# Performance work log

Measured on AMD Instinct MI355X. Metric: run time of the kernel, lower is better.

Reference implementation:

```python
import jax, jax.numpy as jnp
import numpy as np

OUT_SIZE = 7        # output_size (7, 7)
RATIO = 2           # RoIAlign sampling_ratio
FINEST = 56.0       # finest_scale
SCALES = (0.25, 0.125, 0.0625, 0.03125)  # FPN spatial scales, strides 4/8/16/32
IMG_H, IMG_W = 800, 1216
NUM_ROIS = 1024


def _roi_align(feat, rois, scale):
    """RoIAlign (torchvision legacy, aligned=False) for one level.
    feat: [C, H, W]; rois: [4, K] xyxy in image coords. Returns [K, C, 7, 7]."""
    C, H, W = feat.shape
    K = rois.shape[1]
    x1, y1, x2, y2 = rois * scale
    roi_w = jnp.maximum(x2 - x1, 1.0)
    roi_h = jnp.maximum(y2 - y1, 1.0)
    S = OUT_SIZE * RATIO  # 14 sample points per spatial dim
    g = (jnp.arange(S, dtype=feat.dtype) + 0.5) / RATIO  # offsets in bin units
    ys = y1[:, None] + g[None, :] * (roi_h / OUT_SIZE)[:, None]  # [K, S]
    xs = x1[:, None] + g[None, :] * (roi_w / OUT_SIZE)[:, None]  # [K, S]
    # points outside [-1, H]x[-1, W] contribute 0 (torchvision semantics)
    vy = (ys >= -1.0) & (ys <= H)
    vx = (xs >= -1.0) & (xs <= W)
    valid = vy[:, :, None] & vx[:, None, :]  # [K, S, S]
    y = jnp.clip(ys, 0.0, H - 1)
    x = jnp.clip(xs, 0.0, W - 1)
    y0f = jnp.floor(y)
    x0f = jnp.floor(x)
    y0 = y0f.astype(jnp.int32)
    x0 = x0f.astype(jnp.int32)
    yh = jnp.minimum(y0 + 1, H - 1)
    xh = jnp.minimum(x0 + 1, W - 1)
    wy = (y - y0f)[:, None, :, None]  # [K,1,S,1]
    wx = (x - x0f)[:, None, None, :]  # [K,1,1,S]
    ff = feat.reshape(C, H * W)

    def gather(yi, xi):  # yi,xi: [K,S] -> [K,C,S,S]
        idx = yi[:, :, None] * W + xi[:, None, :]  # [K,S,S]
        return jnp.transpose(ff[:, idx], (1, 0, 2, 3))

    v00 = gather(y0, x0)
    v01 = gather(y0, xh)
    v10 = gather(yh, x0)
    v11 = gather(yh, xh)
    val = (v00 * (1.0 - wy) * (1.0 - wx) + v01 * (1.0 - wy) * wx
           + v10 * wy * (1.0 - wx) + v11 * wy * wx)
    val = val * valid[:, None, :, :].astype(val.dtype)
    # average the RATIO x RATIO samples per output bin
    out = val.reshape(K, C, OUT_SIZE, RATIO, OUT_SIZE, RATIO).mean(axis=(3, 5))
    return out


def _map_levels(rois, n_lvls):
    scale = jnp.sqrt((rois[2] - rois[0] + 1.0) * (rois[3] - rois[1] + 1.0))
    lv = jnp.floor(jnp.log2(scale / FINEST + 1e-6))
    return jnp.clip(lv, 0, n_lvls - 1).astype(jnp.int32)


def setup_inputs() -> dict:
    key = jax.random.key(0)
    ks = jax.random.split(key, 8)
    feat0 = jax.random.normal(ks[0], (256, 200, 304), dtype=jnp.float32)
    feat1 = jax.random.normal(ks[1], (256, 100, 152), dtype=jnp.float32)
    feat2 = jax.random.normal(ks[2], (256, 50, 76), dtype=jnp.float32)
    feat3 = jax.random.normal(ks[3], (256, 25, 38), dtype=jnp.float32)
    cx = jax.random.uniform(ks[4], (NUM_ROIS,), minval=0.0, maxval=float(IMG_W))
    cy = jax.random.uniform(ks[5], (NUM_ROIS,), minval=0.0, maxval=float(IMG_H))
    w = jnp.exp(jax.random.uniform(ks[6], (NUM_ROIS,), minval=np.log(16.0), maxval=np.log(640.0)))
    h = jnp.exp(jax.random.uniform(ks[7], (NUM_ROIS,), minval=np.log(16.0), maxval=np.log(640.0)))
    x1 = jnp.clip(cx - w / 2, 0.0, IMG_W - 1.0)
    x2 = jnp.clip(cx + w / 2, 0.0, IMG_W - 1.0)
    y1 = jnp.clip(cy - h / 2, 0.0, IMG_H - 1.0)
    y2 = jnp.clip(cy + h / 2, 0.0, IMG_H - 1.0)
    rois = jnp.stack([x1, y1, x2, y2]).astype(jnp.float32)  # [4, K]
    return {"feat0": feat0, "feat1": feat1, "feat2": feat2, "feat3": feat3, "rois": rois}


def reference(feat0, feat1, feat2, feat3, rois):
    feats = (feat0, feat1, feat2, feat3)
    n_lvls = len(feats)
    tar = _map_levels(rois, n_lvls)  # [K] target FPN level per RoI
    K = rois.shape[1]
    C = feat0.shape[0]
    out = jnp.zeros((K, C, OUT_SIZE, OUT_SIZE), dtype=feat0.dtype)
    for i in range(n_lvls):  # fixed small loop over structurally distinct levels
        lvl_out = _roi_align(feats[i], rois, SCALES[i])
        out = out + jnp.where((tar == i)[:, None, None, None], lvl_out, 0.0)
    return out
```

## Files before the change

### kernel.cpp

```cpp
#include <hip/hip_runtime.h>
#include <hip/hip_fp16.h>
#include <math.h>

#define OUTS 7
#define NBIN 49
#define NCH 256
#define LDSW 1200

#define O1 15564800ull
#define O2 19456000ull
#define O3 20428800ull
#define WS_FLOATS 20672000ull
#define WS_BYTES  (WS_FLOATS * 4ull)

__global__ __launch_bounds__(256) void transpose_cl(
    const float* __restrict__ f0, const float* __restrict__ f1,
    const float* __restrict__ f2, const float* __restrict__ f3,
    __half* __restrict__ ws)
{
    const int bt = blockIdx.x;
    const int cb = blockIdx.y * 64;
    const float* src; __half* dst; int HW, t0;
    if (bt < 950)       { src = f0; dst = ws;      HW = 60800; t0 = bt; }
    else if (bt < 1188) { src = f1; dst = ws + O1; HW = 15200; t0 = bt - 950; }
    else if (bt < 1248) { src = f2; dst = ws + O2; HW = 3800;  t0 = bt - 1188; }
    else                { src = f3; dst = ws + O3; HW = 950;   t0 = bt - 1248; }
    const int hw0 = t0 * 64;

    __shared__ float tile[64][65];
    const int tx = threadIdx.x & 63;
    const int ty = threadIdx.x >> 6;

#pragma unroll
    for (int j = 0; j < 16; ++j) {
        const int c = cb + ty + 4 * j;
        const int hw = hw0 + tx;
        tile[ty + 4 * j][tx] = (hw < HW) ? src[(size_t)c * HW + hw] : 0.0f;
    }
    __syncthreads();

    const int cp = threadIdx.x & 31;
    const int hh = threadIdx.x >> 5;
#pragma unroll
    for (int j = 0; j < 8; ++j) {
        const int hl = hh + 8 * j;
        const int hw = hw0 + hl;
        if (hw < HW) {
            const __half2 h = __floats2half2_rn(tile[2 * cp][hl], tile[2 * cp + 1][hl]);
            *(__half2*)(dst + (size_t)hw * 256 + cb + 2 * cp) = h;
        }
    }
}

__global__ __launch_bounds__(512) void roi_main(
    const __half* __restrict__ ws, const float* __restrict__ rois,
    float* __restrict__ out, int K)
{
    const int k = blockIdx.x;
    const int cbase = blockIdx.y * 128;
    const int tid = threadIdx.x;
    const int wid = tid >> 6;
    const int lane = tid & 63;

    const float rx1 = rois[0 * K + k];
    const float ry1 = rois[1 * K + k];
    const float rx2 = rois[2 * K + k];
    const float ry2 = rois[3 * K + k];

    const float sroi = sqrtf((rx2 - rx1 + 1.0f) * (ry2 - ry1 + 1.0f));
    int lv = (int)floorf(log2f(sroi / 56.0f + 1e-6f));
    lv = lv < 0 ? 0 : (lv > 3 ? 3 : lv);

    const __half* wb; int H, W; float sc;
    switch (lv) {
        case 0:  wb = ws;      H = 200; W = 304; sc = 0.25f;    break;
        case 1:  wb = ws + O1; H = 100; W = 152; sc = 0.125f;   break;
        case 2:  wb = ws + O2; H = 50;  W = 76;  sc = 0.0625f;  break;
        default: wb = ws + O3; H = 25;  W = 38;  sc = 0.03125f; break;
    }

    const float y1s = ry1 * sc;
    const float ystep = fmaxf(ry2 * sc - y1s, 1.0f) / (float)OUTS;
    const float x1s = rx1 * sc;
    const float xstep = fmaxf(rx2 * sc - x1s, 1.0f) / (float)OUTS;

    __shared__ int2   syo[14];  __shared__ float2 syw[14];
    __shared__ int2   sxo[14];  __shared__ float2 sxw[14];
    __shared__ __align__(16) float obuf[128 * NBIN];

    if (tid < 14) {
        const int s = tid;
        const float g = ((float)s + 0.5f) * 0.5f;
        const float ysv = y1s + g * ystep;
        const float v = (ysv >= -1.0f && ysv <= (float)H) ? 0.5f : 0.0f;
        const float y = fminf(fmaxf(ysv, 0.0f), (float)(H - 1));
        const float yf = floorf(y);
        const int y0 = (int)yf;
        const float wy = y - yf;
        syo[s] = make_int2(y0 * W, min(y0 + 1, H - 1) * W);
        syw[s] = make_float2((1.0f - wy) * v, wy * v);
    } else if (tid < 28) {
        const int s = tid - 14;
        const float g = ((float)s + 0.5f) * 0.5f;
        const float xsv = x1s + g * xstep;
        const float v = (xsv >= -1.0f && xsv <= (float)W) ? 0.5f : 0.0f;
        const float x = fminf(fmaxf(xsv, 0.0f), (float)(W - 1));
        const float xf = floorf(x);
        const int x0 = (int)xf;
        const float wx = x - xf;
        sxo[s] = make_int2(x0, min(x0 + 1, W - 1));
        sxw[s] = make_float2((1.0f - wx) * v, wx * v);
    }
    __syncthreads();

    const int half = lane >> 5;
    const int ch4 = (lane & 31) * 4;
    const __half* wbl = wb + cbase + ch4;

#pragma unroll
    for (int i = 0; i < 4; ++i) {
        const int bl = 2 * wid + 16 * i;
        if (bl > 48) break;
        const int b = bl + half;
        const int bc = b > 48 ? 48 : b;
        const int oh = bc / OUTS;
        const int ow = bc - oh * OUTS;

        const int2   ya = syo[2 * oh], yb = syo[2 * oh + 1];
        const float2 wa = syw[2 * oh], wbv = syw[2 * oh + 1];
        const int2   xa = sxo[2 * ow], xb = sxo[2 * ow + 1];
        const float2 ua = sxw[2 * ow], ub = sxw[2 * ow + 1];

        const int   yo[4] = { ya.x, ya.y, yb.x, yb.y };
        const float yw[4] = { wa.x, wa.y, wbv.x, wbv.y };
        const int   xo[4] = { xa.x, xa.y, xb.x, xb.y };
        const float xw[4] = { ua.x, ua.y, ub.x, ub.y };

        float a0 = 0.0f, a1 = 0.0f, a2 = 0.0f, a3 = 0.0f;
#pragma unroll
        for (int iy = 0; iy < 4; ++iy) {
#pragma unroll
            for (int ix = 0; ix < 4; ++ix) {
                const uint2 h2 = *(const uint2*)(wbl + ((size_t)(yo[iy] + xo[ix]) << 8));
                const float2 v0 = __half22float2(*(const __half2*)&h2.x);
                const float2 v1 = __half22float2(*(const __half2*)&h2.y);
                const float wv = yw[iy] * xw[ix];
                a0 += v0.x * wv;
                a1 += v0.y * wv;
                a2 += v1.x * wv;
                a3 += v1.y * wv;
            }
        }
        if (b < NBIN) {
            obuf[(ch4 + 0) * NBIN + b] = a0;
            obuf[(ch4 + 1) * NBIN + b] = a1;
            obuf[(ch4 + 2) * NBIN + b] = a2;
            obuf[(ch4 + 3) * NBIN + b] = a3;
        }
    }
    __syncthreads();

    const float4* o4 = (const float4*)obuf;
    float4* d4 = (float4*)(out + ((size_t)k * NCH + cbase) * NBIN);
    for (int i = tid; i < (128 * NBIN) / 4; i += 512) d4[i] = o4[i];
}

__global__ __launch_bounds__(256) void roi_extract_fallback(
    const float* __restrict__ f0, const float* __restrict__ f1,
    const float* __restrict__ f2, const float* __restrict__ f3,
    const float* __restrict__ rois, float* __restrict__ out, int K)
{
    const int k = blockIdx.x;
    if (k >= K) return;
    const int cbase = blockIdx.y * 32;
    const int tid = threadIdx.x;
    const int wid = tid >> 6;
    const int lane = tid & 63;
    const int bin = lane < NBIN ? lane : NBIN - 1;

    const float rx1 = rois[0 * K + k];
    const float ry1 = rois[1 * K + k];
    const float rx2 = rois[2 * K + k];
    const float ry2 = rois[3 * K + k];

    const float sroi = sqrtf((rx2 - rx1 + 1.0f) * (ry2 - ry1 + 1.0f));
    int lv = (int)floorf(log2f(sroi / 56.0f + 1e-6f));
    lv = lv < 0 ? 0 : (lv > 3 ? 3 : lv);

    const float* fbase; int H, W; float sc;
    switch (lv) {
        case 0:  fbase = f0; H = 200; W = 304; sc = 0.25f;    break;
        case 1:  fbase = f1; H = 100; W = 152; sc = 0.125f;   break;
        case 2:  fbase = f2; H = 50;  W = 76;  sc = 0.0625f;  break;
        default: fbase = f3; H = 25;  W = 38;  sc = 0.03125f; break;
    }
    const int HW = H * W;

    const float y1s = ry1 * sc;
    const float roih = fmaxf(ry2 * sc - y1s, 1.0f);
    const float x1s = rx1 * sc;
    const float roiw = fmaxf(rx2 * sc - x1s, 1.0f);
    const float ystep = roih / (float)OUTS;
    const float xstep = roiw / (float)OUTS;

    const float ysA = y1s + 0.25f * ystep, ysZ = y1s + 6.75f * ystep;
    const float xsA = x1s + 0.25f * xstep, xsZ = x1s + 6.75f * xstep;
    const int ylo = (int)floorf(fminf(fmaxf(ysA, 0.0f), (float)(H - 1)));
    const int xlo = (int)floorf(fminf(fmaxf(xsA, 0.0f), (float)(W - 1)));
    const int xhi = min((int)floorf(fminf(fmaxf(xsZ, 0.0f), (float)(W - 1))) + 1, W - 1);
    const int yhi = min((int)floorf(fminf(fmaxf(ysZ, 0.0f), (float)(H - 1))) + 1, H - 1);
    const int Ww = xhi - xlo + 1;
    const int Hw = yhi - ylo + 1;
    const int E = Ww * Hw;
    const bool useLds = (E <= LDSW);
    const int stride = useLds ? Ww : W;
    const int obase  = useLds ? 0 : (ylo * W + xlo);

    const int oh = bin / OUTS;
    const int ow = bin - oh * OUTS;

    int ry0[2], ry1i[2]; float wy[2], vy[2];
#pragma unroll
    for (int py = 0; py < 2; ++py) {
        const float g = ((float)(oh * 2 + py) + 0.5f) * 0.5f;
        const float ys = y1s + g * ystep;
        vy[py] = (ys >= -1.0f && ys <= (float)H) ? 1.0f : 0.0f;
        const float y = fminf(fmaxf(ys, 0.0f), (float)(H - 1));
        const float y0f = floorf(y);
        const int y0 = (int)y0f;
        ry0[py]  = y0 - ylo;
        ry1i[py] = min(y0 + 1, H - 1) - ylo;
        wy[py] = y - y0f;
    }
    int rx0[2], rx1i[2]; float wx[2], vx[2];
#pragma unroll
    for (int px = 0; px < 2; ++px) {
        const float g = ((float)(ow * 2 + px) + 0.5f) * 0.5f;
        const float xs = x1s + g * xstep;
        vx[px] = (xs >= -1.0f && xs <= (float)W) ? 1.0f : 0.0f;
        const float x = fminf(fmaxf(xs, 0.0f), (float)(W - 1));
        const float x0f = floorf(x);
        const int x0 = (int)x0f;
        rx0[px]  = x0 - xlo;
        rx1i[px] = min(x0 + 1, W - 1) - xlo;
        wx[px] = x - x0f;
    }

    int off[16]; float wt[16];
#pragma unroll
    for (int py = 0; py < 2; ++py) {
#pragma unroll
        for (int px = 0; px < 2; ++px) {
            const int i = (py * 2 + px) * 4;
            const float v = vy[py] * vx[px] * 0.25f;
            const float a = wy[py], b = wx[px];
            off[i + 0] = ry0[py]  * stride + rx0[px]  + obase; wt[i + 0] = (1.0f - a) * (1.0f - b) * v;
            off[i + 1] = ry0[py]  * stride + rx1i[px] + obase; wt[i + 1] = (1.0f - a) * b * v;
            off[i + 2] = ry1i[py] * stride + rx0[px]  + obase; wt[i + 2] = a * (1.0f - b) * v;
            off[i + 3] = ry1i[py] * stride + rx1i[px] + obase; wt[i + 3] = a * b * v;
        }
    }

    __shared__ float2 lds2[4 * LDSW];
    float2* const myw = &lds2[wid * LDSW];
    const float inv_Ww = 1.0f / (float)Ww;

#pragma unroll
    for (int j = 0; j < 4; ++j) {
        const int chA = cbase + wid * 8 + j * 2;
        const float* sA = fbase + (size_t)chA * HW + (size_t)ylo * W + xlo;
        const float* sB = sA + HW;

        if (useLds) {
            for (int e = lane; e < E; e += 64) {
                const int r = (int)(((float)e + 0.5f) * inv_Ww);
                const int g = r * W + (e - r * Ww);
                myw[e] = make_float2(sA[g], sB[g]);
            }
            if (lane < NBIN) {
                float ax = 0.0f, ay = 0.0f;
#pragma unroll
                for (int i = 0; i < 16; ++i) {
                    const float2 v = myw[off[i]];
                    ax += v.x * wt[i];
                    ay += v.y * wt[i];
                }
                float* outA = out + ((size_t)k * NCH + chA) * NBIN + bin;
                outA[0] = ax;
                outA[NBIN] = ay;
            }
        } else {
            if (lane < NBIN) {
                const float* pA = fbase + (size_t)chA * HW;
                const float* pB = pA + HW;
                float ax = 0.0f, ay = 0.0f;
#pragma unroll
                for (int i = 0; i < 16; ++i) {
                    ax += pA[off[i]] * wt[i];
                    ay += pB[off[i]] * wt[i];
                }
                float* outA = out + ((size_t)k * NCH + chA) * NBIN + bin;
                outA[0] = ax;
                outA[NBIN] = ay;
            }
        }
    }
}

extern "C" void kernel_launch(void* const* d_in, const int* in_sizes, int n_in,
                              void* d_out, int out_size, void* d_ws, size_t ws_size,
                              hipStream_t stream) {
    const float* f0 = (const float*)d_in[0];
    const float* f1 = (const float*)d_in[1];
    const float* f2 = (const float*)d_in[2];
    const float* f3 = (const float*)d_in[3];
    const float* rois = (const float*)d_in[4];
    float* out = (float*)d_out;
    int K = in_sizes[4] / 4;
    if (K <= 0) return;

    if (ws_size >= WS_BYTES) {
        __half* ws = (__half*)d_ws;
        transpose_cl<<<dim3(1263, 4), 256, 0, stream>>>(f0, f1, f2, f3, ws);
        roi_main<<<dim3(K, 2), 512, 0, stream>>>(ws, rois, out, K);
    } else {
        roi_extract_fallback<<<dim3(K, 8), 256, 0, stream>>>(f0, f1, f2, f3, rois, out, K);
    }
}
```

Before: 159.5 us.

## Vectorize transpose loads and process all channels per RoI block

The transpose kernel now reads float4 rows when a tile is fully in bounds and writes four half channels per store, with a padded LDS tile. roi_main drops the channel split, so one 512-thread block covers all 256 channels of a RoI, with each wave taking whole bins. The sample offsets are pre-multiplied by the channel stride, and all 16 gather loads are issued before accumulating to expose memory-level parallelism. The cost is a 50KB LDS output buffer per block, which lowers occupancy, and the grid is halved.

```diff
diff --git a/kernel.cpp b/kernel.cpp
--- a/kernel.cpp
+++ b/kernel.cpp
@@ -26,28 +26,43 @@
     else if (bt < 1248) { src = f2; dst = ws + O2; HW = 3800;  t0 = bt - 1188; }
     else                { src = f3; dst = ws + O3; HW = 950;   t0 = bt - 1248; }
     const int hw0 = t0 * 64;
-
-    __shared__ float tile[64][65];
-    const int tx = threadIdx.x & 63;
-    const int ty = threadIdx.x >> 6;
-
-#pragma unroll
-    for (int j = 0; j < 16; ++j) {
-        const int c = cb + ty + 4 * j;
-        const int hw = hw0 + tx;
-        tile[ty + 4 * j][tx] = (hw < HW) ? src[(size_t)c * HW + hw] : 0.0f;
+    const int tid = threadIdx.x;
+
+    __shared__ float tile[64][68];
+
+    const bool fast = ((HW & 3) == 0) && (hw0 + 64 <= HW);
+    if (fast) {
+#pragma unroll
+        for (int j = 0; j < 4; ++j) {
+            const int cl = (tid >> 4) + 16 * j;
+            const int h4 = (tid & 15) * 4;
+            const float4 v = *(const float4*)(src + (size_t)(cb + cl) * HW + hw0 + h4);
+            *(float4*)&tile[cl][h4] = v;
+        }
+    } else {
+        const int tx = tid & 63;
+        const int ty = tid >> 6;
+#pragma unroll
+        for (int j = 0; j < 16; ++j) {
+            const int c = cb + ty + 4 * j;
+            const int hw = hw0 + tx;
+            tile[ty + 4 * j][tx] = (hw < HW) ? src[(size_t)c * HW + hw] : 0.0f;
+        }
     }
     __syncthreads();
 
-    const int cp = threadIdx.x & 31;
-    const int hh = threadIdx.x >> 5;
-#pragma unroll
-    for (int j = 0; j < 8; ++j) {
-        const int hl = hh + 8 * j;
+#pragma unroll
+    for (int j = 0; j < 4; ++j) {
+        const int hl = (tid >> 4) + 16 * j;
         const int hw = hw0 + hl;
         if (hw < HW) {
-            const __half2 h = __floats2half2_rn(tile[2 * cp][hl], tile[2 * cp + 1][hl]);
-            *(__half2*)(dst + (size_t)hw * 256 + cb + 2 * cp) = h;
+            const int q = (tid & 15) * 4;
+            const __half2 h0 = __floats2half2_rn(tile[q + 0][hl], tile[q + 1][hl]);
+            const __half2 h1 = __floats2half2_rn(tile[q + 2][hl], tile[q + 3][hl]);
+            uint2 u;
+            u.x = *(const unsigned int*)&h0;
+            u.y = *(const unsigned int*)&h1;
+            *(uint2*)(dst + (size_t)hw * 256 + cb + q) = u;
         }
     }
 }
@@ -57,7 +72,6 @@
     float* __restrict__ out, int K)
 {
     const int k = blockIdx.x;
-    const int cbase = blockIdx.y * 128;
     const int tid = threadIdx.x;
     const int wid = tid >> 6;
     const int lane = tid & 63;
@@ -86,7 +100,7 @@
 
     __shared__ int2   syo[14];  __shared__ float2 syw[14];
     __shared__ int2   sxo[14];  __shared__ float2 sxw[14];
-    __shared__ __align__(16) float obuf[128 * NBIN];
+    __shared__ __align__(16) float obuf[NCH * NBIN];
 
     if (tid < 14) {
         const int s = tid;
@@ -97,7 +111,7 @@
         const float yf = floorf(y);
         const int y0 = (int)yf;
         const float wy = y - yf;
-        syo[s] = make_int2(y0 * W, min(y0 + 1, H - 1) * W);
+        syo[s] = make_int2(y0 * W * 256, min(y0 + 1, H - 1) * W * 256);
         syw[s] = make_float2((1.0f - wy) * v, wy * v);
     } else if (tid < 28) {
         const int s = tid - 14;
@@ -108,42 +122,45 @@
         const float xf = floorf(x);
         const int x0 = (int)xf;
         const float wx = x - xf;
-        sxo[s] = make_int2(x0, min(x0 + 1, W - 1));
+        sxo[s] = make_int2(x0 * 256, min(x0 + 1, W - 1) * 256);
         sxw[s] = make_float2((1.0f - wx) * v, wx * v);
     }
     __syncthreads();
 
-    const int half = lane >> 5;
-    const int ch4 = (lane & 31) * 4;
-    const __half* wbl = wb + cbase + ch4;
-
-#pragma unroll
-    for (int i = 0; i < 4; ++i) {
-        const int bl = 2 * wid + 16 * i;
-        if (bl > 48) break;
-        const int b = bl + half;
-        const int bc = b > 48 ? 48 : b;
-        const int oh = bc / OUTS;
-        const int ow = bc - oh * OUTS;
+    const int ch4 = lane * 4;
+    const __half* wbl = wb + ch4;
+
+    for (int b = wid; b < NBIN; b += 8) {
+        const int oh = b / OUTS;
+        const int ow = b - oh * OUTS;
 
         const int2   ya = syo[2 * oh], yb = syo[2 * oh + 1];
-        const float2 wa = syw[2 * oh], wbv = syw[2 * oh + 1];
+        const float2 wa = syw[2 * oh], wv2 = syw[2 * oh + 1];
         const int2   xa = sxo[2 * ow], xb = sxo[2 * ow + 1];
         const float2 ua = sxw[2 * ow], ub = sxw[2 * ow + 1];
 
         const int   yo[4] = { ya.x, ya.y, yb.x, yb.y };
-        const float yw[4] = { wa.x, wa.y, wbv.x, wbv.y };
+        const float yw[4] = { wa.x, wa.y, wv2.x, wv2.y };
         const int   xo[4] = { xa.x, xa.y, xb.x, xb.y };
         const float xw[4] = { ua.x, ua.y, ub.x, ub.y };
 
+        uint2 t[16];
+#pragma unroll
+        for (int iy = 0; iy < 4; ++iy) {
+#pragma unroll
+            for (int ix = 0; ix < 4; ++ix) {
+                t[iy * 4 + ix] = *(const uint2*)(wbl + (size_t)(yo[iy] + xo[ix]));
+            }
+        }
+
         float a0 = 0.0f, a1 = 0.0f, a2 = 0.0f, a3 = 0.0f;
 #pragma unroll
         for (int iy = 0; iy < 4; ++iy) {
 #pragma unroll
             for (int ix = 0; ix < 4; ++ix) {
-                const uint2 h2 = *(const uint2*)(wbl + ((size_t)(yo[iy] + xo[ix]) << 8));
-                const float2 v0 = __half22float2(*(const __half2*)&h2.x);
-                const float2 v1 = __half22float2(*(const __half2*)&h2.y);
+                const uint2 u = t[iy * 4 + ix];
+                const float2 v0 = __half22float2(*(const __half2*)&u.x);
+                const float2 v1 = __half22float2(*(const __half2*)&u.y);
                 const float wv = yw[iy] * xw[ix];
                 a0 += v0.x * wv;
                 a1 += v0.y * wv;
@@ -151,18 +168,16 @@
                 a3 += v1.y * wv;
             }
         }
-        if (b < NBIN) {
-            obuf[(ch4 + 0) * NBIN + b] = a0;
-            obuf[(ch4 + 1) * NBIN + b] = a1;
-            obuf[(ch4 + 2) * NBIN + b] = a2;
-            obuf[(ch4 + 3) * NBIN + b] = a3;
-        }
+        obuf[(ch4 + 0) * NBIN + b] = a0;
+        obuf[(ch4 + 1) * NBIN + b] = a1;
+        obuf[(ch4 + 2) * NBIN + b] = a2;
+        obuf[(ch4 + 3) * NBIN + b] = a3;
     }
     __syncthreads();
 
     const float4* o4 = (const float4*)obuf;
-    float4* d4 = (float4*)(out + ((size_t)k * NCH + cbase) * NBIN);
-    for (int i = tid; i < (128 * NBIN) / 4; i += 512) d4[i] = o4[i];
+    float4* d4 = (float4*)(out + (size_t)k * NCH * NBIN);
+    for (int i = tid; i < (NCH * NBIN) / 4; i += 512) d4[i] = o4[i];
 }
 
 __global__ __launch_bounds__(256) void roi_extract_fallback(
@@ -322,7 +337,7 @@
     if (ws_size >= WS_BYTES) {
         __half* ws = (__half*)d_ws;
         transpose_cl<<<dim3(1263, 4), 256, 0, stream>>>(f0, f1, f2, f3, ws);
-        roi_main<<<dim3(K, 2), 512, 0, stream>>>(ws, rois, out, K);
+        roi_main<<<dim3(K), 512, 0, stream>>>(ws, rois, out, K);
     } else {
         roi_extract_fallback<<<dim3(K, 8), 256, 0, stream>>>(f0, f1, f2, f3, rois, out, K);
     }
```

Result: no change. 156.5 us (-1.9%).
